# Kernel optimization log

Hardware: AMD Instinct MI355X
Metric: run time of the kernel (lower is better)

Reference implementation:

```python
import jax, jax.numpy as jnp
import numpy as np

_B, _F, _H, _W = 4, 256, 64, 64
_C, _S = 19, 256  # num_classes, memory-bank half size


def setup_inputs() -> dict:
    key = jax.random.key(0)
    k1, k2, k3, k4, k5 = jax.random.split(key, 5)
    memory_bank = jax.random.normal(k1, (_C, 2 * _S, _F), dtype=jnp.float32)
    pred_rep = jax.random.normal(k2, (_B, _F, _H, _W), dtype=jnp.float32)
    labels = jax.random.randint(k3, (_B, _H, _W), 0, _C)
    mask = jax.random.randint(k4, (_B, _H, _W), 0, 2).astype(bool)
    which_memory = jax.random.randint(k5, (_B, _H, _W), 0, 2)
    return {
        "memory_bank": memory_bank,
        "pred_rep": pred_rep,
        "labels": labels,
        "mask": mask,
        "which_memory": which_memory,
        "num_classes": _C,
    }


def reference(memory_bank, pred_rep, labels, mask, which_memory, num_classes, temp=0.5):
    eps = 1e-12
    C, twoS, F = memory_bank.shape
    S = twoS // 2
    # pixels-first layout: [P, F]
    feats = jnp.transpose(pred_rep, (0, 2, 3, 1)).reshape(-1, F)
    lab = labels.reshape(-1)
    msk = mask.reshape(-1)
    wm = which_memory.reshape(-1)
    mem = memory_bank.reshape(-1, F)  # [C*2S, F]
    fn = jnp.linalg.norm(feats, axis=1)  # [P]
    mn = jnp.linalg.norm(mem, axis=1)    # [C*2S]
    cos = (feats @ mem.T) / (fn[:, None] * mn[None, :])
    E = jnp.exp(cos / temp)              # [P, C*2S]
    Eb = E.reshape(-1, C, twoS)
    total = Eb.sum(axis=(1, 2))          # [P] sum over full bank
    block_sum = Eb.sum(axis=2)           # [P, C]
    loss = jnp.float32(0.0)
    class_count = jnp.float32(0.0)
    for i in range(num_classes):
        choice = msk & (lab == i)
        cnt = choice.sum()
        down = total - block_sum[:, i]   # negatives = all other classes
        block = Eb[:, i, :]              # [P, 2S] positives for class i
        contrib = jnp.float32(0.0)
        for net in range(2):
            sel = choice & (wm == 1 - net)
            pos = block[:, :S] if net == 0 else block[:, S:]
            term = -jnp.log(pos / (pos + down[:, None] + eps) + eps)
            contrib = contrib + jnp.where(sel[:, None], term, 0.0).sum()
        denom = jnp.maximum(cnt, 1).astype(jnp.float32) * S
        loss = loss + jnp.where(cnt > 0, contrib / denom, 0.0)
        class_count = class_count + (cnt > 0).astype(jnp.float32)
    return loss / jnp.maximum(class_count, 1.0)
```

## Files before the change

### kernel.cpp

```cpp
#include <hip/hip_runtime.h>
#include <hip/hip_bf16.h>
#include <math.h>

#define B_ 4
#define F_ 256
#define C_ 19
#define S_ 256
#define N_ 16384
#define M_ 9728
#define MT_ 38
#define PREP_PRED 256
#define PREP_MEM 2432
#define PREP_BUCKET0 2688
#define GEMM_BLKS 512
#define P2_BLOCKS (C_ * 16)

typedef __bf16 bf16_t;
typedef bf16_t bf16x8 __attribute__((ext_vector_type(8)));
typedef float floatx4 __attribute__((ext_vector_type(4)));

#define AS1 __attribute__((address_space(1)))
#define AS3 __attribute__((address_space(3)))

__device__ inline size_t fragoff(int row, int f) {
    return ((size_t)((row >> 4) * 8 + (f >> 5))) * 512
         + (size_t)((((f >> 3) & 3) * 128) + ((row & 15) * 8) + (f & 7));
}

__global__ __launch_bounds__(256) void k_prep(const float* __restrict__ pred,
                                              const float* __restrict__ mem,
                                              __hip_bfloat16* __restrict__ A16f,
                                              __hip_bfloat16* __restrict__ B16,
                                              const int* __restrict__ labels,
                                              const int* __restrict__ mask,
                                              int* __restrict__ ccnt,
                                              int* __restrict__ pix) {
    int bid = blockIdx.x;
    int t = threadIdx.x;
    if (bid < PREP_PRED) {
        __shared__ float part[4][64];
        __shared__ float invf_s[64];
        int b = bid >> 6, hw0 = (bid & 63) * 64;
        int j = t & 63, q = t >> 6;
        int n0 = b * 4096 + hw0;

        const float* base = pred + ((size_t)b * F_ + q * 64) * 4096 + hw0 + j;
        float v[64];
        float s = 0.f;
        #pragma unroll
        for (int i = 0; i < 64; ++i) {
            float x = base[(size_t)i * 4096];
            v[i] = x;
            s += x * x;
        }
        part[q][j] = s;
        __syncthreads();
        if (t < 64) invf_s[t] = 1.0f / sqrtf(part[0][t] + part[1][t] + part[2][t] + part[3][t]);
        __syncthreads();
        float invf = invf_s[j];
        #pragma unroll
        for (int c = 0; c < 8; ++c) {
            int f = q * 64 + c * 8;
            __hip_bfloat16 tmp[8];
            #pragma unroll
            for (int u = 0; u < 8; ++u) tmp[u] = __float2bfloat16(v[c * 8 + u] * invf);
            *(float4*)&A16f[fragoff(n0 + j, f)] = *(float4*)tmp;
        }
    } else if (bid < PREP_BUCKET0) {
        int row  = (bid - PREP_PRED) * 4 + (t >> 6);
        int lane = t & 63;
        float4 a = ((const float4*)(mem + (size_t)row * F_))[lane];
        float s = a.x*a.x + a.y*a.y + a.z*a.z + a.w*a.w;
        #pragma unroll
        for (int off = 32; off; off >>= 1) s += __shfl_xor(s, off, 64);
        float invm = 1.0f / sqrtf(s);
        __hip_bfloat16 tmp[4];
        tmp[0] = __float2bfloat16(a.x * invm);
        tmp[1] = __float2bfloat16(a.y * invm);
        tmp[2] = __float2bfloat16(a.z * invm);
        tmp[3] = __float2bfloat16(a.w * invm);
        *(float2*)&B16[fragoff(row, lane * 4)] = *(float2*)tmp;
    } else {
        __shared__ int hist[C_], base_s[C_], cur[C_];
        int n0 = (bid - PREP_BUCKET0) * 256;
        if (t < C_) { hist[t] = 0; cur[t] = 0; }
        __syncthreads();
        int myc = labels[n0 + t];
        int mym = mask[n0 + t];
        if (mym) atomicAdd(&hist[myc], 1);
        __syncthreads();
        if (t < C_) base_s[t] = atomicAdd(&ccnt[t], hist[t]);
        __syncthreads();
        if (mym) {
            int o = atomicAdd(&cur[myc], 1);
            pix[myc * N_ + base_s[myc] + o] = n0 + t;
        }
    }
}

__global__ __launch_bounds__(512, 4) void k_pass1(const __hip_bfloat16* __restrict__ A16f,
                                                  const __hip_bfloat16* __restrict__ B16,
                                                  float* __restrict__ totpart) {
    __shared__ __hip_bfloat16 As[128 * 256];
    __shared__ float totals_s[2][4][128];
    int bid = blockIdx.x;
    int t = threadIdx.x;
    int w = t >> 6, lane = t & 63;
    int xcd = bid & 7, j = bid >> 3;
    int nt = ((j & 15) << 3) | xcd;
    int chunk = j >> 4;
    int n0 = nt * 128;
    int nh = w & 1, mq = w >> 1;

    {
        const __hip_bfloat16* src = A16f + ((size_t)n0 << 8) + w * 4096 + lane * 8;
        __hip_bfloat16* dst = &As[w * 4096];
        #pragma unroll
        for (int i = 0; i < 8; ++i)
            __builtin_amdgcn_global_load_lds((const AS1 unsigned int*)(src + i * 512),
                                             (AS3 unsigned int*)(dst + i * 512), 16, 0, 0);
    }
    __syncthreads();

    int colL = lane & 15, rgrp = (lane >> 4) * 4;
    int p = 0;
    for (int mt = chunk; mt < MT_; mt += 4, p ^= 1) {
        floatx4 acc[4][4];
        #pragma unroll
        for (int i = 0; i < 4; ++i)
            #pragma unroll
            for (int j2 = 0; j2 < 4; ++j2) acc[i][j2] = (floatx4){0.f, 0.f, 0.f, 0.f};

        const bf16x8* Bp = (const bf16x8*)B16 + ((size_t)(mt * 16 + mq * 4) * 8) * 64 + lane;

        #pragma unroll
        for (int kt = 0; kt < 8; ++kt) {
            bf16x8 af[4], bfr[4];
            #pragma unroll
            for (int ni = 0; ni < 4; ++ni)
                af[ni] = *(const bf16x8*)&As[((nh * 4 + ni) * 8 + kt) * 512 + lane * 8];
            #pragma unroll
            for (int mi = 0; mi < 4; ++mi)
                bfr[mi] = Bp[(size_t)(mi * 8 + kt) * 64];
            __builtin_amdgcn_s_setprio(1);
            #pragma unroll
            for (int ni = 0; ni < 4; ++ni)
                #pragma unroll
                for (int mi = 0; mi < 4; ++mi)
                    acc[ni][mi] = __builtin_amdgcn_mfma_f32_16x16x32_bf16(af[ni], bfr[mi], acc[ni][mi], 0, 0, 0);
            __builtin_amdgcn_s_setprio(0);
        }

        float racc[4][4];
        #pragma unroll
        for (int ni = 0; ni < 4; ++ni)
            #pragma unroll
            for (int r = 0; r < 4; ++r) racc[ni][r] = 0.f;
        #pragma unroll
        for (int ni = 0; ni < 4; ++ni)
            #pragma unroll
            for (int mi = 0; mi < 4; ++mi)
                #pragma unroll
                for (int r = 0; r < 4; ++r)
                    racc[ni][r] += __expf(2.0f * acc[ni][mi][r]);

        #pragma unroll
        for (int ni = 0; ni < 4; ++ni)
            #pragma unroll
            for (int r = 0; r < 4; ++r) {
                float s = racc[ni][r];
                s += __shfl_xor(s, 1, 64);
                s += __shfl_xor(s, 2, 64);
                s += __shfl_xor(s, 4, 64);
                s += __shfl_xor(s, 8, 64);
                if (colL == 0) totals_s[p][mq][nh * 64 + ni * 16 + rgrp + r] = s;
            }
        __syncthreads();
        if (t < 128)
            totpart[(size_t)mt * N_ + n0 + t] =
                totals_s[p][0][t] + totals_s[p][1][t] + totals_s[p][2][t] + totals_s[p][3][t];
    }
}

__global__ __launch_bounds__(512) void k_pass2(const __hip_bfloat16* __restrict__ A16f,
                                               const __hip_bfloat16* __restrict__ B16,
                                               const int* __restrict__ ccnt,
                                               const int* __restrict__ pix,
                                               const float* __restrict__ totpart,
                                               const int* __restrict__ wmem,
                                               float* __restrict__ class_sum,
                                               int* __restrict__ done,
                                               float* __restrict__ out) {
    __shared__ __hip_bfloat16 As[64 * 256];
    __shared__ int pidx_s[64];
    __shared__ float tot_s[64];
    __shared__ int wm_s[64];
    __shared__ float bsum_s[8][64];
    __shared__ float wsum_s[8][64];
    __shared__ float down_s[64];
    __shared__ float term_s[64];

    int c = blockIdx.x, tile = blockIdx.y;
    int cnt = ccnt[c];
    int t = threadIdx.x, ws = t >> 6, lane = t & 63;

    if (tile * 64 >= cnt) {
        if (t == 0) {
            __threadfence();
            int old = atomicAdd(done, 1);
            if (old == P2_BLOCKS - 1) {
                float loss = 0.f, kc = 0.f;
                for (int cc = 0; cc < C_; ++cc) {
                    int cn = ccnt[cc];
                    float sc = atomicAdd(&class_sum[cc], 0.f);
                    if (cn > 0) { loss += sc / ((float)cn * (float)S_); kc += 1.f; }
                }
                out[0] = loss / fmaxf(kc, 1.f);
            }
        }
        return;
    }

    if (t < 64) {
        int i = tile * 64 + t;
        int p = pix[c * N_ + (i < cnt ? i : 0)];
        pidx_s[t] = p;
        wm_s[t]   = wmem[p];
    }
    __syncthreads();

    {
        int px = t >> 3, g = t & 7;
        int p = pidx_s[px];
        float s = 0.f;
        for (int i = g; i < MT_; i += 8) s += totpart[(size_t)i * N_ + p];
        s += __shfl_xor(s, 1, 64);
        s += __shfl_xor(s, 2, 64);
        s += __shfl_xor(s, 4, 64);
        if (g == 0) tot_s[px] = s;
    }

    #pragma unroll
    for (int s2 = 0; s2 < 4; ++s2) {
        int g = t + 512 * s2;
        int row = g >> 5, f = (g & 31) * 8;
        float4 v = *(const float4*)&A16f[fragoff(pidx_s[row], f)];
        *(float4*)&As[fragoff(row, f)] = v;
    }
    __syncthreads();

    floatx4 acc[4][4];
    #pragma unroll
    for (int i = 0; i < 4; ++i)
        #pragma unroll
        for (int j = 0; j < 4; ++j) acc[i][j] = (floatx4){0.f, 0.f, 0.f, 0.f};

    const bf16x8* Bp = (const bf16x8*)B16 + ((size_t)(c * 32 + ws * 4) * 8) * 64 + lane;
    #pragma unroll
    for (int kt = 0; kt < 8; ++kt) {
        bf16x8 af[4], bfr[4];
        #pragma unroll
        for (int ni = 0; ni < 4; ++ni)
            af[ni] = *(const bf16x8*)&As[(ni * 8 + kt) * 512 + lane * 8];
        #pragma unroll
        for (int mi = 0; mi < 4; ++mi) bfr[mi] = Bp[(size_t)(mi * 8 + kt) * 64];
        #pragma unroll
        for (int ni = 0; ni < 4; ++ni)
            #pragma unroll
            for (int mi = 0; mi < 4; ++mi)
                acc[ni][mi] = __builtin_amdgcn_mfma_f32_16x16x32_bf16(af[ni], bfr[mi], acc[ni][mi], 0, 0, 0);
    }

    int colL = lane & 15, rgrp = (lane >> 4) * 4;
    float Ev[4][4][4];
    #pragma unroll
    for (int ni = 0; ni < 4; ++ni)
        #pragma unroll
        for (int mi = 0; mi < 4; ++mi)
            #pragma unroll
            for (int r = 0; r < 4; ++r)
                Ev[ni][mi][r] = __expf(2.0f * acc[ni][mi][r]);

    #pragma unroll
    for (int ni = 0; ni < 4; ++ni)
        #pragma unroll
        for (int r = 0; r < 4; ++r) {
            float s = Ev[ni][0][r] + Ev[ni][1][r] + Ev[ni][2][r] + Ev[ni][3][r];
            s += __shfl_xor(s, 1, 64);
            s += __shfl_xor(s, 2, 64);
            s += __shfl_xor(s, 4, 64);
            s += __shfl_xor(s, 8, 64);
            if (colL == 0) bsum_s[ws][ni * 16 + rgrp + r] = s;
        }
    __syncthreads();
    if (t < 64) {
        float bs = 0.f;
        #pragma unroll
        for (int w2 = 0; w2 < 8; ++w2) bs += bsum_s[w2][t];
        down_s[t] = tot_s[t] - bs;
    }
    __syncthreads();

    #pragma unroll
    for (int ni = 0; ni < 4; ++ni)
        #pragma unroll
        for (int r = 0; r < 4; ++r) {
            int row = ni * 16 + rgrp + r;
            bool sel = (wm_s[row] == 1) ? (ws < 4) : (ws >= 4);
            float tt = 0.f;
            if (sel) {
                float dwn = down_s[row];
                #pragma unroll
                for (int mi = 0; mi < 4; ++mi) {
                    float pv = Ev[ni][mi][r];
                    tt += -logf(pv / (pv + dwn + 1e-12f) + 1e-12f);
                }
            }
            tt += __shfl_xor(tt, 1, 64);
            tt += __shfl_xor(tt, 2, 64);
            tt += __shfl_xor(tt, 4, 64);
            tt += __shfl_xor(tt, 8, 64);
            if (colL == 0) wsum_s[ws][row] = tt;
        }
    __syncthreads();
    if (t < 64) {
        int i = tile * 64 + t;
        float s = 0.f;
        if (i < cnt) {
            #pragma unroll
            for (int w2 = 0; w2 < 8; ++w2) s += wsum_s[w2][t];
        }
        term_s[t] = s;
    }
    __syncthreads();
    if (t < 64) {
        float s = term_s[t];
        #pragma unroll
        for (int off = 1; off < 64; off <<= 1) s += __shfl_xor(s, off, 64);
        if (t == 0) {
            atomicAdd(&class_sum[c], s);
            __threadfence();
            int old = atomicAdd(done, 1);
            if (old == P2_BLOCKS - 1) {
                float loss = 0.f, kc = 0.f;
                for (int cc = 0; cc < C_; ++cc) {
                    int cn = ccnt[cc];
                    float sc = atomicAdd(&class_sum[cc], 0.f);
                    if (cn > 0) { loss += sc / ((float)cn * (float)S_); kc += 1.f; }
                }
                out[0] = loss / fmaxf(kc, 1.f);
            }
        }
    }
}

extern "C" void kernel_launch(void* const* d_in, const int* in_sizes, int n_in,
                              void* d_out, int out_size, void* d_ws, size_t ws_size,
                              hipStream_t stream) {
    const float* mem    = (const float*)d_in[0];
    const float* pred   = (const float*)d_in[1];
    const int*   labels = (const int*)  d_in[2];
    const int*   mask   = (const int*)  d_in[3];
    const int*   wmem   = (const int*)  d_in[4];
    float* out = (float*)d_out;

    float* ws = (float*)d_ws;
    float* totpart   = ws;
    int*   ctrl      = (int*)(ws + 622592);
    int*   ccnt      = ctrl;
    float* class_sum = (float*)(ctrl + 19);
    int*   done      = ctrl + 38;
    int*   pix       = (int*)(ws + 622640);
    __hip_bfloat16* A16f = (__hip_bfloat16*)(ws + 933936);
    __hip_bfloat16* B16  = (__hip_bfloat16*)(ws + 3031088);

    hipMemsetAsync(ctrl, 0, 40 * sizeof(int), stream);

    k_prep<<<PREP_BUCKET0 + 64, 256, 0, stream>>>(pred, mem, A16f, B16,
                                                  labels, mask, ccnt, pix);

    k_pass1<<<GEMM_BLKS, 512, 0, stream>>>(A16f, B16, totpart);

    dim3 g2(C_, 16);
    k_pass2<<<g2, 512, 0, stream>>>(A16f, B16, ccnt, pix, totpart, wmem,
                                    class_sum, done, out);
}
```

Before: 196.8 us.

## Write per-wave partial totals directly to global and halve prep pixel tile

In pass1, each wave now writes its row-sum partials straight to a 4x larger global partial buffer instead of staging them in shared memory and reducing across waves after a __syncthreads. The trailing sync becomes a bare s_barrier. Pass2 sums 152 partials per pixel instead of 38. Separately, the pred-normalisation prep uses 512 blocks of 32 pixels, which cuts per-thread register arrays from 64 to 32 floats. The cost is more global writes from pass1 and more scattered reads in pass2.

```diff
diff --git a/kernel.cpp b/kernel.cpp
--- a/kernel.cpp
+++ b/kernel.cpp
@@ -9,9 +9,8 @@
 #define N_ 16384
 #define M_ 9728
 #define MT_ 38
-#define PREP_PRED 256
-#define PREP_MEM 2432
-#define PREP_BUCKET0 2688
+#define PREP_PRED 512
+#define PREP_BUCKET0 2944
 #define GEMM_BLKS 512
 #define P2_BLOCKS (C_ * 16)
 
@@ -38,29 +37,34 @@
     int bid = blockIdx.x;
     int t = threadIdx.x;
     if (bid < PREP_PRED) {
-        __shared__ float part[4][64];
-        __shared__ float invf_s[64];
-        int b = bid >> 6, hw0 = (bid & 63) * 64;
-        int j = t & 63, q = t >> 6;
+        __shared__ float part[8][32];
+        __shared__ float invf_s[32];
+        int b = bid >> 7, hw0 = (bid & 127) * 32;
+        int j = t & 31, q = t >> 5;
         int n0 = b * 4096 + hw0;
 
-        const float* base = pred + ((size_t)b * F_ + q * 64) * 4096 + hw0 + j;
-        float v[64];
+        const float* base = pred + ((size_t)b * F_ + q * 32) * 4096 + hw0 + j;
+        float v[32];
         float s = 0.f;
         #pragma unroll
-        for (int i = 0; i < 64; ++i) {
+        for (int i = 0; i < 32; ++i) {
             float x = base[(size_t)i * 4096];
             v[i] = x;
             s += x * x;
         }
         part[q][j] = s;
         __syncthreads();
-        if (t < 64) invf_s[t] = 1.0f / sqrtf(part[0][t] + part[1][t] + part[2][t] + part[3][t]);
+        if (t < 32) {
+            float sum = 0.f;
+            #pragma unroll
+            for (int qq = 0; qq < 8; ++qq) sum += part[qq][t];
+            invf_s[t] = 1.0f / sqrtf(sum);
+        }
         __syncthreads();
         float invf = invf_s[j];
         #pragma unroll
-        for (int c = 0; c < 8; ++c) {
-            int f = q * 64 + c * 8;
+        for (int c = 0; c < 4; ++c) {
+            int f = q * 32 + c * 8;
             __hip_bfloat16 tmp[8];
             #pragma unroll
             for (int u = 0; u < 8; ++u) tmp[u] = __float2bfloat16(v[c * 8 + u] * invf);
@@ -100,9 +104,8 @@
 
 __global__ __launch_bounds__(512, 4) void k_pass1(const __hip_bfloat16* __restrict__ A16f,
                                                   const __hip_bfloat16* __restrict__ B16,
-                                                  float* __restrict__ totpart) {
+                                                  float* __restrict__ totpart4) {
     __shared__ __hip_bfloat16 As[128 * 256];
-    __shared__ float totals_s[2][4][128];
     int bid = blockIdx.x;
     int t = threadIdx.x;
     int w = t >> 6, lane = t & 63;
@@ -123,8 +126,7 @@
     __syncthreads();
 
     int colL = lane & 15, rgrp = (lane >> 4) * 4;
-    int p = 0;
-    for (int mt = chunk; mt < MT_; mt += 4, p ^= 1) {
+    for (int mt = chunk; mt < MT_; mt += 4) {
         floatx4 acc[4][4];
         #pragma unroll
         for (int i = 0; i < 4; ++i)
@@ -164,6 +166,7 @@
                 for (int r = 0; r < 4; ++r)
                     racc[ni][r] += __expf(2.0f * acc[ni][mi][r]);
 
+        float* outp = totpart4 + (size_t)(mt * 4 + mq) * N_ + n0 + nh * 64;
         #pragma unroll
         for (int ni = 0; ni < 4; ++ni)
             #pragma unroll
@@ -173,12 +176,9 @@
                 s += __shfl_xor(s, 2, 64);
                 s += __shfl_xor(s, 4, 64);
                 s += __shfl_xor(s, 8, 64);
-                if (colL == 0) totals_s[p][mq][nh * 64 + ni * 16 + rgrp + r] = s;
+                if (colL == 0) outp[ni * 16 + rgrp + r] = s;
             }
-        __syncthreads();
-        if (t < 128)
-            totpart[(size_t)mt * N_ + n0 + t] =
-                totals_s[p][0][t] + totals_s[p][1][t] + totals_s[p][2][t] + totals_s[p][3][t];
+        __builtin_amdgcn_s_barrier();
     }
 }
 
@@ -186,7 +186,7 @@
                                                const __hip_bfloat16* __restrict__ B16,
                                                const int* __restrict__ ccnt,
                                                const int* __restrict__ pix,
-                                               const float* __restrict__ totpart,
+                                               const float* __restrict__ totpart4,
                                                const int* __restrict__ wmem,
                                                float* __restrict__ class_sum,
                                                int* __restrict__ done,
@@ -233,7 +233,7 @@
         int px = t >> 3, g = t & 7;
         int p = pidx_s[px];
         float s = 0.f;
-        for (int i = g; i < MT_; i += 8) s += totpart[(size_t)i * N_ + p];
+        for (int i = g; i < MT_ * 4; i += 8) s += totpart4[(size_t)i * N_ + p];
         s += __shfl_xor(s, 1, 64);
         s += __shfl_xor(s, 2, 64);
         s += __shfl_xor(s, 4, 64);
@@ -365,23 +365,23 @@
     float* out = (float*)d_out;
 
     float* ws = (float*)d_ws;
-    float* totpart   = ws;
-    int*   ctrl      = (int*)(ws + 622592);
+    float* totpart4  = ws;
+    int*   ctrl      = (int*)(ws + 2490368);
     int*   ccnt      = ctrl;
     float* class_sum = (float*)(ctrl + 19);
     int*   done      = ctrl + 38;
-    int*   pix       = (int*)(ws + 622640);
-    __hip_bfloat16* A16f = (__hip_bfloat16*)(ws + 933936);
-    __hip_bfloat16* B16  = (__hip_bfloat16*)(ws + 3031088);
+    int*   pix       = (int*)(ws + 2490416);
+    __hip_bfloat16* A16f = (__hip_bfloat16*)(ws + 2801712);
+    __hip_bfloat16* B16  = (__hip_bfloat16*)(ws + 4898864);
 
     hipMemsetAsync(ctrl, 0, 40 * sizeof(int), stream);
 
     k_prep<<<PREP_BUCKET0 + 64, 256, 0, stream>>>(pred, mem, A16f, B16,
                                                   labels, mask, ccnt, pix);
 
-    k_pass1<<<GEMM_BLKS, 512, 0, stream>>>(A16f, B16, totpart);
+    k_pass1<<<GEMM_BLKS, 512, 0, stream>>>(A16f, B16, totpart4);
 
     dim3 g2(C_, 16);
-    k_pass2<<<g2, 512, 0, stream>>>(A16f, B16, ccnt, pix, totpart, wmem,
+    k_pass2<<<g2, 512, 0, stream>>>(A16f, B16, ccnt, pix, totpart4, wmem,
                                     class_sum, done, out);
 }
```

Result: slower. 201.4 us (+2.4%).

## Compute pass-1 totals only for masked pixels via compacted class-ordered slots

Applied to the files above, without the earlier changes.

Pass 1 now builds its pixel panels from the class-bucketed list of masked pixels rather than all pixels. The full-bank exp-sum GEMM therefore only runs for pixels that contribute to the loss, roughly half of them. Blocks are split across panels and column chunks according to the runtime count. Pass 2 reads the totals by compacted slot index. Rows are now gathered per pixel instead of loaded with a contiguous direct-to-LDS copy, and each thread serially scans the class counts to find its pixel.

```diff
diff --git a/kernel.cpp b/kernel.cpp
--- a/kernel.cpp
+++ b/kernel.cpp
@@ -10,7 +10,6 @@
 #define M_ 9728
 #define MT_ 38
 #define PREP_PRED 256
-#define PREP_MEM 2432
 #define PREP_BUCKET0 2688
 #define GEMM_BLKS 512
 #define P2_BLOCKS (C_ * 16)
@@ -100,31 +99,56 @@
 
 __global__ __launch_bounds__(512, 4) void k_pass1(const __hip_bfloat16* __restrict__ A16f,
                                                   const __hip_bfloat16* __restrict__ B16,
+                                                  const int* __restrict__ ccnt,
+                                                  const int* __restrict__ pix,
                                                   float* __restrict__ totpart) {
     __shared__ __hip_bfloat16 As[128 * 256];
     __shared__ float totals_s[2][4][128];
+    __shared__ int pidx_s[128];
     int bid = blockIdx.x;
     int t = threadIdx.x;
     int w = t >> 6, lane = t & 63;
-    int xcd = bid & 7, j = bid >> 3;
-    int nt = ((j & 15) << 3) | xcd;
-    int chunk = j >> 4;
-    int n0 = nt * 128;
     int nh = w & 1, mq = w >> 1;
 
-    {
-        const __hip_bfloat16* src = A16f + ((size_t)n0 << 8) + w * 4096 + lane * 8;
-        __hip_bfloat16* dst = &As[w * 4096];
-        #pragma unroll
-        for (int i = 0; i < 8; ++i)
-            __builtin_amdgcn_global_load_lds((const AS1 unsigned int*)(src + i * 512),
-                                             (AS3 unsigned int*)(dst + i * 512), 16, 0, 0);
+    int cnt_all = 0;
+    #pragma unroll
+    for (int cc = 0; cc < C_; ++cc) cnt_all += ccnt[cc];
+    int nt_total = (cnt_all + 127) >> 7;
+    if (nt_total == 0) return;
+    int nchunk = GEMM_BLKS / nt_total;
+    if (nchunk > MT_) nchunk = MT_;
+    if (bid >= nt_total * nchunk) return;
+    int panel = bid % nt_total;
+    int chunk = bid / nt_total;
+    int slot0 = panel * 128;
+
+    if (t < 128) {
+        int slot = slot0 + t;
+        int run = 0, pixid = 0;
+        #pragma unroll
+        for (int cc = 0; cc < C_; ++cc) {
+            int cn = ccnt[cc];
+            if (slot >= run && slot < run + cn) pixid = pix[cc * N_ + slot - run];
+            run += cn;
+        }
+        if (slot >= cnt_all) pixid = 0;
+        pidx_s[t] = pixid;
+    }
+    __syncthreads();
+
+    #pragma unroll
+    for (int s = 0; s < 8; ++s) {
+        int k = t + 512 * s;
+        int row = ((k >> 9) << 4) | (k & 15);
+        int f   = ((k >> 6) & 7) * 32 + ((k >> 4) & 3) * 8;
+        float4 v = *(const float4*)&A16f[fragoff(pidx_s[row], f)];
+        ((float4*)As)[k] = v;
     }
     __syncthreads();
 
     int colL = lane & 15, rgrp = (lane >> 4) * 4;
     int p = 0;
-    for (int mt = chunk; mt < MT_; mt += 4, p ^= 1) {
+    for (int mt = chunk; mt < MT_; mt += nchunk, p ^= 1) {
         floatx4 acc[4][4];
         #pragma unroll
         for (int i = 0; i < 4; ++i)
@@ -175,9 +199,9 @@
                 s += __shfl_xor(s, 8, 64);
                 if (colL == 0) totals_s[p][mq][nh * 64 + ni * 16 + rgrp + r] = s;
             }
-        __syncthreads();
+        asm volatile("s_waitcnt lgkmcnt(0)\n\ts_barrier" ::: "memory");
         if (t < 128)
-            totpart[(size_t)mt * N_ + n0 + t] =
+            totpart[(size_t)mt * N_ + slot0 + t] =
                 totals_s[p][0][t] + totals_s[p][1][t] + totals_s[p][2][t] + totals_s[p][3][t];
     }
 }
@@ -221,6 +245,11 @@
         return;
     }
 
+    int pre = 0;
+    #pragma unroll
+    for (int cc = 0; cc < C_; ++cc) if (cc < c) pre += ccnt[cc];
+    int slot0 = pre + tile * 64;
+
     if (t < 64) {
         int i = tile * 64 + t;
         int p = pix[c * N_ + (i < cnt ? i : 0)];
@@ -231,9 +260,8 @@
 
     {
         int px = t >> 3, g = t & 7;
-        int p = pidx_s[px];
         float s = 0.f;
-        for (int i = g; i < MT_; i += 8) s += totpart[(size_t)i * N_ + p];
+        for (int i = g; i < MT_; i += 8) s += totpart[(size_t)i * N_ + slot0 + px];
         s += __shfl_xor(s, 1, 64);
         s += __shfl_xor(s, 2, 64);
         s += __shfl_xor(s, 4, 64);
@@ -379,7 +407,7 @@
     k_prep<<<PREP_BUCKET0 + 64, 256, 0, stream>>>(pred, mem, A16f, B16,
                                                   labels, mask, ccnt, pix);
 
-    k_pass1<<<GEMM_BLKS, 512, 0, stream>>>(A16f, B16, totpart);
+    k_pass1<<<GEMM_BLKS, 512, 0, stream>>>(A16f, B16, ccnt, pix, totpart);
 
     dim3 g2(C_, 16);
     k_pass2<<<g2, 512, 0, stream>>>(A16f, B16, ccnt, pix, totpart, wmem,
```

Measured after the change: 177.2 us. 9.9% less time.
